# Optimization experiments

Hardware: AMD Instinct MI355X
Metric: run time of the kernel (lower is better)

Reference implementation:

```python
import jax, jax.numpy as jnp
import numpy as np

B, OBS, ACT = 16384, 39, 4
D = 400            # backbone_hidden[-1] == expert_hidden[-1] == task_queries_dim
NE, NT = 8, 10     # num_experts, num_tasks


def setup_inputs() -> dict:
    key = jax.random.key(0)
    ks = jax.random.split(key, 20)
    g = lambda k, shp, fan: jax.random.normal(k, shp, dtype=jnp.float32) / np.sqrt(fan)
    return {
        "obs": jax.random.normal(ks[0], (B, OBS), dtype=jnp.float32),
        "act": jax.random.normal(ks[1], (B, ACT), dtype=jnp.float32),
        "task": jax.random.randint(ks[2], (B,), 0, NT),
        # backbone mlp: [obs+act, 400, 400], relu after each layer
        "bb_w1": g(ks[3], (OBS + ACT, D), OBS + ACT), "bb_b1": jnp.zeros((D,), jnp.float32),
        "bb_w2": g(ks[4], (D, D), D), "bb_b2": jnp.zeros((D,), jnp.float32),
        # 8 expert mlps, stacked: [400 -> 400 -> 400], relu after each layer
        "ex_w1": g(ks[5], (NE, D, D), D), "ex_b1": jnp.zeros((NE, D), jnp.float32),
        "ex_w2": g(ks[6], (NE, D, D), D), "ex_b2": jnp.zeros((NE, D), jnp.float32),
        # attention params
        "key_mat": g(ks[7], (NE, D, D), D),
        "value_mat": g(ks[8], (NE, D, D), D),
        "task_queries": jax.random.normal(ks[9], (NT, D), dtype=jnp.float32),
        # tower mlp: [400, 400, 400, 1], relu on hidden layers, identity output
        "tw_w1": g(ks[10], (D, D), D), "tw_b1": jnp.zeros((D,), jnp.float32),
        "tw_w2": g(ks[11], (D, D), D), "tw_b2": jnp.zeros((D,), jnp.float32),
        "tw_w3": g(ks[12], (D, 1), D), "tw_b3": jnp.zeros((1,), jnp.float32),
    }


def reference(obs, act, task, bb_w1, bb_b1, bb_w2, bb_b2,
              ex_w1, ex_b1, ex_w2, ex_b2,
              key_mat, value_mat, task_queries,
              tw_w1, tw_b1, tw_w2, tw_b2, tw_w3, tw_b3):
    x = jnp.concatenate([obs, act], axis=-1)                       # [B, obs+act]
    h = jax.nn.relu(x @ bb_w1 + bb_b1)
    h = jax.nn.relu(h @ bb_w2 + bb_b2)                             # [B, D]
    # all experts as one batched GEMM: e[n, b, :] = expert_n(h[b])
    e = jax.nn.relu(jnp.einsum('bi,nij->nbj', h, ex_w1) + ex_b1[:, None, :])
    e = jax.nn.relu(jnp.einsum('nbi,nij->nbj', e, ex_w2) + ex_b2[:, None, :])  # [NE, B, D]
    # per-expert key/value projections (einsum 'nij,nj->ni' batched over b)
    vals = jnp.einsum('nij,nbj->bni', value_mat, e)                # [B, NE, D]
    keys = jnp.einsum('nij,nbj->bni', key_mat, e)                  # [B, NE, D]
    q = task_queries[task]                                         # [B, D]
    scores = jnp.einsum('bni,bi->bn', keys, q)                     # [B, NE]
    w = jax.nn.softmax(scores, axis=-1)                            # softmax over experts
    tower_in = jnp.einsum('bn,bni->bi', w, vals)                   # [B, D]
    t = jax.nn.relu(tower_in @ tw_w1 + tw_b1)
    t = jax.nn.relu(t @ tw_w2 + tw_b2)
    qval = t @ tw_w3 + tw_b3                                       # [B, 1]
    return jnp.squeeze(qval, -1)                                   # [B]
```

## Files before the change

### kernel.cpp

```cpp
#include <hip/hip_runtime.h>

typedef _Float16 f16;
typedef f16 f16x8 __attribute__((ext_vector_type(8)));
typedef float f32x4 __attribute__((ext_vector_type(4)));

#define NB 16384
#define D 400
#define DP 416
#define NEXP 8
#define NTASK 10
#define NKT 13

#define MEMFENCE asm volatile("" ::: "memory")
#define BAR() do{ MEMFENCE; __builtin_amdgcn_s_barrier(); MEMFENCE; }while(0)
#define VM(N) asm volatile("s_waitcnt vmcnt(" #N ")" ::: "memory")
#define LGKM0 asm volatile("s_waitcnt lgkmcnt(0)" ::: "memory")

static __device__ __forceinline__ f32x4 mfma16x32(f16x8 a, f16x8 b, f32x4 c){
  return __builtin_amdgcn_mfma_f32_16x16x32_f16(a, b, c, 0, 0, 0);
}
static __device__ __forceinline__ void g2l(const void* g, void* l){
  __builtin_amdgcn_global_load_lds((const __attribute__((address_space(1))) void*)g,
      (__attribute__((address_space(3))) void*)l, 16, 0, 0);
}
static __device__ __forceinline__ f16x8 scale8(f16x8 a, f16 s){
  f16x8 r;
  #pragma unroll
  for (int e=0;e<8;e++) r[e] = a[e]*s;
  return r;
}

static __device__ __forceinline__ void stage_duo(const char* wbase, char* lds, int kt,
                                                 int t0, int dd, int h, int lane){
  const int r = lane >> 3, c = lane & 7, cg = c ^ r;
  g2l(wbase + (size_t)((t0 + dd*2 + (cg>>2))*16 + h*8 + r)*832 + (size_t)kt*64 + (cg&3)*16,
      lds + dd*2048 + h*1024);
}
static __device__ __forceinline__ f16x8 rdB(const f16* buf, int dloc, int t, int lhi, int l15){
  return *(const f16x8*)(buf + dloc*1024 + l15*64 + ((((t*4+lhi) ^ (l15&7)))<<3));
}
static __device__ __forceinline__ f16x8 rdL(const f16* lact, int r, int kt, int lhi){
  int q = kt*4 + lhi;
  int c = (q < 48) ? (q ^ (r&7)) : q;
  return *(const f16x8*)(lact + r*416 + (c<<3));
}
static __device__ __forceinline__ int lact_idx(int r, int col){
  int q = col >> 3;
  int c = (q < 48) ? (q ^ (r&7)) : q;
  return r*416 + (c<<3) + (col&7);
}
static __device__ __forceinline__ void stageB4(const char* wb, char* buf, int kt,
                                               int wv, int lane){
  for (int u = wv; u < 26; u += 4) stage_duo(wb, buf, kt, 0, u>>1, u&1, lane);
}


__global__ void k_build_x(const float* __restrict__ obs, const float* __restrict__ act,
                          f16* __restrict__ x)
{
  int idx = blockIdx.x*256 + threadIdx.x;
  int b = idx >> 6, c = idx & 63;
  float v = 0.f;
  if (c < 39) v = obs[b*39 + c];
  else if (c < 43) v = act[b*4 + (c - 39)];
  x[idx] = (f16)v;
}

__global__ void k_transpose_all(
    const float* __restrict__ bb_w1, const float* __restrict__ bb_w2,
    const float* __restrict__ ex_w1, const float* __restrict__ ex_w2,
    const float* __restrict__ tw_w1, const float* __restrict__ tw_w2,
    f16* __restrict__ bbw1T, f16* __restrict__ bbw2T,
    f16* __restrict__ exw1T, f16* __restrict__ exw2T,
    f16* __restrict__ tw1T,  f16* __restrict__ tw2T)
{
  __shared__ float t[32][33];
  const int z = blockIdx.z;
  const float* in; f16* out; int K = D;
  if (z == 0){ in = bb_w1; out = bbw1T; K = 43; }
  else if (z == 1){ in = bb_w2; out = bbw2T; }
  else if (z < 10){ in = ex_w1 + (size_t)(z-2)*D*D;  out = exw1T + (size_t)(z-2)*DP*DP; }
  else if (z < 18){ in = ex_w2 + (size_t)(z-10)*D*D; out = exw2T + (size_t)(z-10)*DP*DP; }
  else if (z == 18){ in = tw_w1; out = tw1T; }
  else { in = tw_w2; out = tw2T; }
  int tx = threadIdx.x & 31, ty = threadIdx.x >> 5;
  int n0 = blockIdx.x*32, k0 = blockIdx.y*32;
  #pragma unroll
  for (int r=0;r<4;r++){
    int k = k0 + ty + r*8, nn = n0 + tx;
    t[ty + r*8][tx] = (k < K && nn < D) ? in[(size_t)k*D + nn] : 0.f;
  }
  __syncthreads();
  #pragma unroll
  for (int r=0;r<4;r++){
    int nn = n0 + ty + r*8, kp = k0 + tx;
    if (nn < DP && kp < DP) out[(size_t)nn*DP + kp] = (f16)t[tx][ty + r*8];
  }
}

__global__ void k_val_pad(const float* __restrict__ in, f16* __restrict__ out)
{
  int idx = blockIdx.x*256 + threadIdx.x;
  if (idx >= NEXP*DP*DP) return;
  int c = idx % DP, r = (idx / DP) % DP, n = idx / (DP*DP);
  float v = (r < D && c < D) ? in[((size_t)n*D + r)*D + c] : 0.f;
  out[idx] = (f16)v;
}

__global__ void k_kq(const float* __restrict__ key_mat, const float* __restrict__ tq,
                     float* __restrict__ kq)
{
  __shared__ float kcol[D*32];
  __shared__ float tqs[NTASK*D];
  const int n = blockIdx.x, cb = blockIdx.y, tid = threadIdx.x;
  const int c0 = cb*32;
  const float* km = key_mat + (size_t)n*D*D;
  for (int idx=tid; idx<NTASK*D; idx+=256) tqs[idx] = tq[idx];
  for (int idx=tid; idx<D*32; idx+=256){
    int i = idx>>5, c = idx&31;
    int col = c0 + c;
    kcol[idx] = (col < D) ? km[(size_t)i*D + col] : 0.f;
  }
  __syncthreads();
  const int c = tid & 31, tg = tid >> 5;
  #pragma unroll
  for (int rep=0; rep<2; rep++){
    int t = tg + rep*8;
    if (t < NTASK){
      float acc = 0.f;
      for (int i=0;i<D;i++) acc += kcol[i*32+c] * tqs[t*D+i];
      int col = c0 + c;
      if (col < DP) kq[((size_t)n*NTASK + t)*DP + col] = acc;
    }
  }
}


#define MFMA26(a0_, a1_, BUF) do {                                              \
    __builtin_amdgcn_s_setprio(1);                                              \
    _Pragma("unroll")                                                           \
    for (int j=0;j<13;j++){                                                     \
      int tj = ch*13 + j;                                                       \
      f16x8 b = rdB((BUF), tj>>1, tj&1, lhi, l15);                              \
      acc[0][j] = mfma16x32((a0_), b, acc[0][j]);                               \
      acc[1][j] = mfma16x32((a1_), b, acc[1][j]);                               \
    }                                                                           \
    __builtin_amdgcn_s_setprio(0);                                              \
  } while(0)

#define MFMA13(a0_, BUF) do {                                                   \
    __builtin_amdgcn_s_setprio(1);                                              \
    _Pragma("unroll")                                                           \
    for (int j=0;j<13;j++){                                                     \
      int tj = ch*13 + j;                                                       \
      f16x8 b = rdB((BUF), tj>>1, tj&1, lhi, l15);                              \
      acc[j] = mfma16x32((a0_), b, acc[j]);                                     \
    }                                                                           \
    __builtin_amdgcn_s_setprio(0);                                              \
  } while(0)

#define STAGE_W(wb_, buf_, p_, full_) do{                                       \
    int tot_ = (full_) ? 52 : 26;                                               \
    for (int u = wv; u < tot_; u += 4){                                         \
      int kh_ = (u >= 26) ? 1 : 0, uu_ = u - (kh_ ? 26 : 0);                    \
      stage_duo((wb_), (char*)(buf_)[kh_], 2*(p_)+kh_, 0, uu_>>1, uu_&1, lane); \
    }                                                                           \
  } while(0)

__global__ __launch_bounds__(256,2) void k_experts(
    const f16* __restrict__ h16, const f16* __restrict__ w1T, const float* __restrict__ b1s,
    const f16* __restrict__ w2T, const float* __restrict__ b2s,
    f16* __restrict__ e16, const float* __restrict__ kqg, const int* __restrict__ task,
    float* __restrict__ scores)
{
  __shared__ f16 bufB[13*1024];
  __shared__ f16 lact[64*416];
  float (*psum)[2] = (float(*)[2])lact;
  const int tid = threadIdx.x, lane = tid & 63, wv = tid >> 6;
  const int l15 = lane & 15, lhi = lane >> 4;
  const int rh = wv >> 1, ch = wv & 1;
  const int n = blockIdx.x;
  const int rowbase = blockIdx.y * 64;
  const int K0 = ((blockIdx.x + blockIdx.y) & 1) * 7;
  const f32x4 Z4 = {0,0,0,0};
  f32x4 acc[2][13];

  const char* wb1 = (const char*)(w1T + (size_t)n*DP*DP);
  const char* wb2 = (const char*)(w2T + (size_t)n*DP*DP);
  const f16* Ab = h16 + (size_t)(rowbase + rh*32 + l15)*DP;

  #pragma unroll
  for (int j=0;j<13;j++){ acc[0][j]=Z4; acc[1][j]=Z4; }
  f16x8 a0 = *(const f16x8*)(Ab + K0*32 + lhi*8);
  f16x8 a1 = *(const f16x8*)(Ab + 16*DP + K0*32 + lhi*8);
  stageB4(wb1, (char*)bufB, K0, wv, lane);
  for (int kt=0; kt<NKT; kt++){
    VM(0); BAR();
    MFMA26(a0, a1, bufB);
    BAR();
    if (kt < NKT-1){
      int kn = kt + 1 + K0; if (kn >= NKT) kn -= NKT;
      a0 = *(const f16x8*)(Ab + kn*32 + lhi*8);
      a1 = *(const f16x8*)(Ab + 16*DP + kn*32 + lhi*8);
      stageB4(wb1, (char*)bufB, kn, wv, lane);
    }
  }
  stageB4(wb2, (char*)bufB, K0, wv, lane);
  #pragma unroll
  for (int j=0;j<13;j++){
    int col = (ch*13+j)*16 + l15;
    float bv = (col<D)? b1s[n*D+col] : 0.f;
    #pragma unroll
    for (int ar=0;ar<2;ar++)
      #pragma unroll
      for (int rr=0;rr<4;rr++){
        float v = acc[ar][j][rr] + bv; v = v>0.f?v:0.f;
        lact[lact_idx(rh*32+ar*16+lhi*4+rr, col)] = (f16)v;
      }
  }
  LGKM0;

  #pragma unroll
  for (int j=0;j<13;j++){ acc[0][j]=Z4; acc[1][j]=Z4; }
  for (int kt=0; kt<NKT; kt++){
    int ka = kt + K0; if (ka >= NKT) ka -= NKT;
    VM(0); BAR();
    f16x8 x0 = rdL(lact, rh*32 + l15, ka, lhi);
    f16x8 x1 = rdL(lact, rh*32 + 16 + l15, ka, lhi);
    MFMA26(x0, x1, bufB);
    BAR();
    if (kt < NKT-1){
      int kn = kt + 1 + K0; if (kn >= NKT) kn -= NKT;
      stageB4(wb2, (char*)bufB, kn, wv, lane);
    }
  }
  const float* kqp[2][4];
  const float* kqb = kqg + (size_t)n*NTASK*DP;
  #pragma unroll
  for (int ar=0;ar<2;ar++)
    #pragma unroll
    for (int rr=0;rr<4;rr++){
      int grow = rowbase + rh*32 + ar*16 + lhi*4 + rr;
      kqp[ar][rr] = kqb + (size_t)task[grow]*DP;
    }
  float p_[2][4] = {{0,0,0,0},{0,0,0,0}};
  #pragma unroll
  for (int j=0;j<13;j++){
    int col = (ch*13+j)*16 + l15;
    float bv = (col<D)? b2s[n*D+col] : 0.f;
    #pragma unroll
    for (int ar=0;ar<2;ar++)
      #pragma unroll
      for (int rr=0;rr<4;rr++){
        float v = acc[ar][j][rr] + bv; v = v>0.f?v:0.f;
        e16[((size_t)n*NB + rowbase + rh*32+ar*16+lhi*4+rr)*DP + col] = (f16)v;
        p_[ar][rr] += v * kqp[ar][rr][col];
      }
  }
  #pragma unroll
  for (int ar=0;ar<2;ar++)
    #pragma unroll
    for (int rr=0;rr<4;rr++){
      float p = p_[ar][rr];
      p += __shfl_xor(p, 1, 64);
      p += __shfl_xor(p, 2, 64);
      p += __shfl_xor(p, 4, 64);
      p += __shfl_xor(p, 8, 64);
      if (l15 == 0) psum[rh*32+ar*16+lhi*4+rr][ch] = p;
    }
  LGKM0; BAR();
  if (tid < 64) scores[(size_t)(rowbase + tid)*NEXP + n] = psum[tid][0] + psum[tid][1];
}

__global__ __launch_bounds__(256,2) void k_backbone(
    const f16* __restrict__ x, const f16* __restrict__ w1T, const float* __restrict__ b1,
    const f16* __restrict__ w2T, const float* __restrict__ b2, f16* __restrict__ h16)
{
  __shared__ f16 bufB[2][13*1024];
  __shared__ f16 lact[32*416];
  const int tid = threadIdx.x, lane = tid & 63, wv = tid >> 6;
  const int l15 = lane & 15, lhi = lane >> 4;
  const int rh = wv >> 1, ch = wv & 1;
  const int rowbase = blockIdx.x * 32;
  const int P0 = (blockIdx.x & 1) * 3;
  const f32x4 Z4 = {0,0,0,0};
  f32x4 acc[13];

  const f16* Ab = x + (size_t)(rowbase + rh*16 + l15)*64;

  #pragma unroll
  for (int j=0;j<13;j++) acc[j]=Z4;
  STAGE_W((const char*)w1T, bufB, 0, 1);
  f16x8 a0 = *(const f16x8*)(Ab + lhi*8);
  f16x8 a1 = *(const f16x8*)(Ab + 32 + lhi*8);
  VM(0); BAR();
  MFMA13(a0, bufB[0]);
  MFMA13(a1, bufB[1]);
  BAR();
  { int pa0 = P0; STAGE_W((const char*)w2T, bufB, pa0, pa0 != 6); }
  #pragma unroll
  for (int j=0;j<13;j++){
    int col = (ch*13+j)*16 + l15;
    float bv = (col<D)? b1[col] : 0.f;
    #pragma unroll
    for (int rr=0;rr<4;rr++){
      float v = acc[j][rr] + bv; v = v>0.f?v:0.f;
      lact[lact_idx(rh*16+lhi*4+rr, col)] = (f16)v;
    }
  }
  LGKM0;

  #pragma unroll
  for (int j=0;j<13;j++) acc[j]=Z4;
  for (int p=0; p<7; p++){
    int pa = p + P0; if (pa >= 7) pa -= 7;
    VM(0); BAR();
    f16x8 x0 = rdL(lact, rh*16 + l15, 2*pa, lhi);
    MFMA13(x0, bufB[0]);
    if (pa != 6){
      f16x8 x1 = rdL(lact, rh*16 + l15, 2*pa+1, lhi);
      MFMA13(x1, bufB[1]);
    }
    BAR();
    if (p < 6){
      int pn = p + 1 + P0; if (pn >= 7) pn -= 7;
      STAGE_W((const char*)w2T, bufB, pn, pn != 6);
    }
  }
  #pragma unroll
  for (int j=0;j<13;j++){
    int col = (ch*13+j)*16 + l15;
    float bv = (col<D)? b2[col] : 0.f;
    #pragma unroll
    for (int rr=0;rr<4;rr++){
      float v = acc[j][rr] + bv; v = v>0.f?v:0.f;
      h16[(size_t)(rowbase + rh*16+lhi*4+rr)*DP + col] = (f16)v;
    }
  }
}

__global__ __launch_bounds__(256,2) void k_attn(
    const f16* __restrict__ e16, const f16* __restrict__ valT,
    const float* __restrict__ scores, f16* __restrict__ ti16)
{
  __shared__ f16 buf[2][7*1024];
  __shared__ float wsm[64*NEXP];
  const int tid = threadIdx.x, lane = tid & 63, wv = tid >> 6;
  const int l15 = lane & 15, lhi = lane >> 4;
  const int rg = wv >> 1, cg = wv & 1;
  const int cb = blockIdx.x;
  const int rowbase = blockIdx.y * 64;
  const int nd = cb ? 6 : 7;
  const int ntw = cb ? 6 : 7;
  const int t0 = cb * 14;
  const int S0 = ((blockIdx.x + blockIdx.y) & 1) * 28;
  const f32x4 Z4 = {0,0,0,0};
  f32x4 acc[2][7];
  #pragma unroll
  for (int a=0;a<2;a++)
    #pragma unroll
    for (int j=0;j<7;j++) acc[a][j]=Z4;

  if (tid < 64){
    const float* sr = scores + (size_t)(rowbase + tid)*NEXP;
    float s[8]; float m = -1e30f;
    #pragma unroll
    for (int k=0;k<8;k++){ s[k]=sr[k]; m = fmaxf(m, s[k]); }
    float sum = 0.f;
    #pragma unroll
    for (int k=0;k<8;k++){ s[k] = expf(s[k]-m); sum += s[k]; }
    float inv = 1.f/sum;
    #pragma unroll
    for (int k=0;k<8;k++) wsm[tid*NEXP + k] = s[k]*inv;
  }

  #define STAGE_A(n_, p_) do {                                                  \
    const char* vb_ = (const char*)(valT + (size_t)(n_)*DP*DP);                 \
    int nu_ = nd*2, tot_ = ((p_)<6) ? nd*4 : nd*2;                              \
    for (int u = wv; u < tot_; u += 4){                                         \
      int kh_ = (u >= nu_) ? 1 : 0, uu_ = u - (kh_ ? nu_ : 0);                  \
      stage_duo(vb_, (char*)buf[kh_], 2*(p_)+kh_, t0, uu_>>1, uu_&1, lane);     \
    }                                                                           \
  } while(0)

  #define LDA_A(n_, kt_, ar_) \
    (*(const f16x8*)(e16 + ((size_t)(n_)*NB + rowbase + rg*32 + (ar_)*16 + l15)*DP + (kt_)*32 + lhi*8))

  const int nS = S0 / 7;
  STAGE_A(nS, 0);
  f16x8 aC00 = LDA_A(nS,0,0), aC01 = LDA_A(nS,0,1);
  f16x8 aC10 = LDA_A(nS,1,0), aC11 = LDA_A(nS,1,1);
  LGKM0;

  for (int s=0;s<NEXP*7;s++){
    int sa = s + S0; if (sa >= NEXP*7) sa -= NEXP*7;
    int n = sa / 7, p = sa % 7;
    VM(0); BAR();
    f16 w0 = (f16)wsm[(rg*32      + l15)*NEXP + n];
    f16 w1 = (f16)wsm[(rg*32 + 16 + l15)*NEXP + n];
    {
      f16x8 as0 = scale8(aC00, w0), as1 = scale8(aC01, w1);
      __builtin_amdgcn_s_setprio(1);
      #pragma unroll
      for (int j=0;j<7;j++) if (j<ntw){
        int tl = cg*ntw + j;
        f16x8 b = rdB(buf[0], tl>>1, tl&1, lhi, l15);
        acc[0][j] = mfma16x32(as0, b, acc[0][j]);
        acc[1][j] = mfma16x32(as1, b, acc[1][j]);
      }
      __builtin_amdgcn_s_setprio(0);
    }
    if (p < 6){
      f16x8 as0 = scale8(aC10, w0), as1 = scale8(aC11, w1);
      __builtin_amdgcn_s_setprio(1);
      #pragma unroll
      for (int j=0;j<7;j++) if (j<ntw){
        int tl = cg*ntw + j;
        f16x8 b = rdB(buf[1], tl>>1, tl&1, lhi, l15);
        acc[0][j] = mfma16x32(as0, b, acc[0][j]);
        acc[1][j] = mfma16x32(as1, b, acc[1][j]);
      }
      __builtin_amdgcn_s_setprio(0);
    }
    BAR();
    if (s < NEXP*7 - 1){
      int sa2 = sa + 1; if (sa2 >= NEXP*7) sa2 -= NEXP*7;
      int n2 = sa2 / 7, p2 = sa2 % 7;
      STAGE_A(n2, p2);
      aC00 = LDA_A(n2, 2*p2,   0); aC01 = LDA_A(n2, 2*p2,   1);
      if (p2 < 6){ aC10 = LDA_A(n2, 2*p2+1, 0); aC11 = LDA_A(n2, 2*p2+1, 1); }
    }
  }
  #pragma unroll
  for (int ar=0;ar<2;ar++)
    #pragma unroll
    for (int j=0;j<7;j++) if (j<ntw){
      int col = (t0 + cg*ntw + j)*16 + l15;
      #pragma unroll
      for (int rr=0;rr<4;rr++)
        ti16[(size_t)(rowbase + rg*32 + ar*16 + lhi*4 + rr)*DP + col] = (f16)acc[ar][j][rr];
    }
}

__global__ __launch_bounds__(256,2) void k_mlp3(
    const f16* __restrict__ ti16,
    const f16* __restrict__ tw1T, const float* __restrict__ tb1,
    const f16* __restrict__ tw2T, const float* __restrict__ tb2,
    const float* __restrict__ tw3, const float* __restrict__ tb3,
    float* __restrict__ out)
{
  __shared__ f16 bufB[2][13*1024];
  __shared__ f16 lact[32*416];
  float (*psum)[2] = (float(*)[2])lact;
  const int tid = threadIdx.x, lane = tid & 63, wv = tid >> 6;
  const int l15 = lane & 15, lhi = lane >> 4;
  const int rh = wv >> 1, ch = wv & 1;
  const int rowbase = blockIdx.x * 32;
  const int P0 = (blockIdx.x & 1) * 3;
  const f32x4 Z4 = {0,0,0,0};
  f32x4 acc[13];

  const f16* Ab = ti16 + (size_t)(rowbase + rh*16 + l15)*DP;

  #pragma unroll
  for (int j=0;j<13;j++) acc[j]=Z4;
  STAGE_W((const char*)tw1T, bufB, P0, P0 != 6);
  f16x8 a0 = *(const f16x8*)(Ab + (2*P0)*32 + lhi*8);
  f16x8 a1 = (P0 != 6) ? *(const f16x8*)(Ab + (2*P0+1)*32 + lhi*8) : a0;
  for (int p=0; p<7; p++){
    int pa = p + P0; if (pa >= 7) pa -= 7;
    VM(0); BAR();
    MFMA13(a0, bufB[0]);
    if (pa != 6) MFMA13(a1, bufB[1]);
    BAR();
    if (p < 6){
      int pn = p + 1 + P0; if (pn >= 7) pn -= 7;
      STAGE_W((const char*)tw1T, bufB, pn, pn != 6);
      a0 = *(const f16x8*)(Ab + (2*pn)*32 + lhi*8);
      if (pn != 6) a1 = *(const f16x8*)(Ab + (2*pn+1)*32 + lhi*8);
    }
  }
  { int pa0 = P0; STAGE_W((const char*)tw2T, bufB, pa0, pa0 != 6); }
  #pragma unroll
  for (int j=0;j<13;j++){
    int col = (ch*13+j)*16 + l15;
    float bv = (col<D)? tb1[col] : 0.f;
    #pragma unroll
    for (int rr=0;rr<4;rr++){
      float v = acc[j][rr] + bv; v = v>0.f?v:0.f;
      lact[lact_idx(rh*16+lhi*4+rr, col)] = (f16)v;
    }
  }
  LGKM0;

  #pragma unroll
  for (int j=0;j<13;j++) acc[j]=Z4;
  for (int p=0; p<7; p++){
    int pa = p + P0; if (pa >= 7) pa -= 7;
    VM(0); BAR();
    f16x8 x0 = rdL(lact, rh*16 + l15, 2*pa, lhi);
    MFMA13(x0, bufB[0]);
    if (pa != 6){
      f16x8 x1 = rdL(lact, rh*16 + l15, 2*pa+1, lhi);
      MFMA13(x1, bufB[1]);
    }
    BAR();
    if (p < 6){
      int pn = p + 1 + P0; if (pn >= 7) pn -= 7;
      STAGE_W((const char*)tw2T, bufB, pn, pn != 6);
    }
  }
  float p_[4] = {0,0,0,0};
  #pragma unroll
  for (int j=0;j<13;j++){
    int col = (ch*13+j)*16 + l15;
    float bv = (col<D)? tb2[col] : 0.f;
    float w3 = (col<D)? tw3[col] : 0.f;
    #pragma unroll
    for (int rr=0;rr<4;rr++){
      float v = acc[j][rr] + bv; v = v>0.f?v:0.f;
      p_[rr] += v * w3;
    }
  }
  #pragma unroll
  for (int rr=0;rr<4;rr++){
    float p = p_[rr];
    p += __shfl_xor(p, 1, 64);
    p += __shfl_xor(p, 2, 64);
    p += __shfl_xor(p, 4, 64);
    p += __shfl_xor(p, 8, 64);
    if (l15 == 0) psum[rh*16+lhi*4+rr][ch] = p;
  }
  LGKM0; BAR();
  if (tid < 32) out[rowbase + tid] = psum[tid][0] + psum[tid][1] + tb3[0];
}


extern "C" void kernel_launch(void* const* d_in, const int* in_sizes, int n_in,
                              void* d_out, int out_size, void* d_ws, size_t ws_size,
                              hipStream_t stream)
{
  const float* obs     = (const float*)d_in[0];
  const float* act     = (const float*)d_in[1];
  const int*   task    = (const int*)  d_in[2];
  const float* bb_w1   = (const float*)d_in[3];
  const float* bb_b1   = (const float*)d_in[4];
  const float* bb_w2   = (const float*)d_in[5];
  const float* bb_b2   = (const float*)d_in[6];
  const float* ex_w1   = (const float*)d_in[7];
  const float* ex_b1   = (const float*)d_in[8];
  const float* ex_w2   = (const float*)d_in[9];
  const float* ex_b2   = (const float*)d_in[10];
  const float* key_mat = (const float*)d_in[11];
  const float* val_mat = (const float*)d_in[12];
  const float* tq      = (const float*)d_in[13];
  const float* tw_w1   = (const float*)d_in[14];
  const float* tw_b1   = (const float*)d_in[15];
  const float* tw_w2   = (const float*)d_in[16];
  const float* tw_b2   = (const float*)d_in[17];
  const float* tw_w3   = (const float*)d_in[18];
  const float* tw_b3   = (const float*)d_in[19];

  char* ws = (char*)d_ws;
  size_t off = 0;
  auto alloc = [&](size_t bytes){ void* p = ws + off; off += (bytes + 255) & ~(size_t)255; return p; };
  f16*   x16   = (f16*)  alloc((size_t)NB*64*2);
  f16*   h16   = (f16*)  alloc((size_t)NB*DP*2);
  f16*   e16   = (f16*)  alloc((size_t)NEXP*NB*DP*2);
  f16*   ti16  = (f16*)  alloc((size_t)NB*DP*2);
  float* scors = (float*)alloc((size_t)NB*NEXP*4);
  float* kq    = (float*)alloc((size_t)NEXP*NTASK*DP*4);
  f16*   bbw1T = (f16*)  alloc((size_t)DP*DP*2);
  f16*   bbw2T = (f16*)  alloc((size_t)DP*DP*2);
  f16*   exw1T = (f16*)  alloc((size_t)NEXP*DP*DP*2);
  f16*   exw2T = (f16*)  alloc((size_t)NEXP*DP*DP*2);
  f16*   valT  = (f16*)  alloc((size_t)NEXP*DP*DP*2);
  f16*   tw1T  = (f16*)  alloc((size_t)DP*DP*2);
  f16*   tw2T  = (f16*)  alloc((size_t)DP*DP*2);
  (void)ws_size; (void)in_sizes; (void)n_in; (void)out_size;

  k_build_x<<<NB*64/256, 256, 0, stream>>>(obs, act, x16);
  k_transpose_all<<<dim3(13,13,20), 256, 0, stream>>>(
      bb_w1, bb_w2, ex_w1, ex_w2, tw_w1, tw_w2,
      bbw1T, bbw2T, exw1T, exw2T, tw1T, tw2T);
  k_val_pad<<<(NEXP*DP*DP + 255)/256, 256, 0, stream>>>(val_mat, valT);
  k_kq<<<dim3(NEXP, 13), 256, 0, stream>>>(key_mat, tq, kq);

  k_backbone<<<NB/32, 256, 0, stream>>>(x16, bbw1T, bb_b1, bbw2T, bb_b2, h16);
  k_experts<<<dim3(NEXP, NB/64), 256, 0, stream>>>(h16, exw1T, ex_b1, exw2T, ex_b2,
                                                   e16, kq, task, scors);
  k_attn<<<dim3(2, NB/64), 256, 0, stream>>>(e16, valT, scors, ti16);
  k_mlp3<<<NB/32, 256, 0, stream>>>(ti16, tw1T, tw_b1, tw2T, tw_b2, tw_w3, tw_b3,
                                    (float*)d_out);
}
```

Before: 364.1 us.

## Use 512-thread blocks in experts and attention kernels with 16 rows per wave

Doubles the block size of k_experts and k_attn from 256 to 512 threads. Each wave now computes one 16-row MFMA tile instead of two, which halves its accumulator registers. Weight staging is spread over 8 waves. The aim is more waves in flight to hide latency and less register pressure per wave. The cost is that each B fragment read from LDS now feeds half as many MFMAs, and more waves take part in every barrier.

```diff
diff --git a/kernel.cpp b/kernel.cpp
--- a/kernel.cpp
+++ b/kernel.cpp
@@ -52,6 +52,10 @@
 static __device__ __forceinline__ void stageB4(const char* wb, char* buf, int kt,
                                                int wv, int lane){
   for (int u = wv; u < 26; u += 4) stage_duo(wb, buf, kt, 0, u>>1, u&1, lane);
+}
+static __device__ __forceinline__ void stageB8(const char* wb, char* buf, int kt,
+                                               int wv, int lane){
+  for (int u = wv; u < 26; u += 8) stage_duo(wb, buf, kt, 0, u>>1, u&1, lane);
 }
 
 
@@ -136,18 +140,6 @@
 }
 
 
-#define MFMA26(a0_, a1_, BUF) do {                                              \
-    __builtin_amdgcn_s_setprio(1);                                              \
-    _Pragma("unroll")                                                           \
-    for (int j=0;j<13;j++){                                                     \
-      int tj = ch*13 + j;                                                       \
-      f16x8 b = rdB((BUF), tj>>1, tj&1, lhi, l15);                              \
-      acc[0][j] = mfma16x32((a0_), b, acc[0][j]);                               \
-      acc[1][j] = mfma16x32((a1_), b, acc[1][j]);                               \
-    }                                                                           \
-    __builtin_amdgcn_s_setprio(0);                                              \
-  } while(0)
-
 #define MFMA13(a0_, BUF) do {                                                   \
     __builtin_amdgcn_s_setprio(1);                                              \
     _Pragma("unroll")                                                           \
@@ -167,7 +159,7 @@
     }                                                                           \
   } while(0)
 
-__global__ __launch_bounds__(256,2) void k_experts(
+__global__ __launch_bounds__(512,2) void k_experts(
     const f16* __restrict__ h16, const f16* __restrict__ w1T, const float* __restrict__ b1s,
     const f16* __restrict__ w2T, const float* __restrict__ b2s,
     f16* __restrict__ e16, const float* __restrict__ kqg, const int* __restrict__ task,
@@ -183,91 +175,80 @@
   const int rowbase = blockIdx.y * 64;
   const int K0 = ((blockIdx.x + blockIdx.y) & 1) * 7;
   const f32x4 Z4 = {0,0,0,0};
-  f32x4 acc[2][13];
+  f32x4 acc[13];
 
   const char* wb1 = (const char*)(w1T + (size_t)n*DP*DP);
   const char* wb2 = (const char*)(w2T + (size_t)n*DP*DP);
-  const f16* Ab = h16 + (size_t)(rowbase + rh*32 + l15)*DP;
-
-  #pragma unroll
-  for (int j=0;j<13;j++){ acc[0][j]=Z4; acc[1][j]=Z4; }
+  const f16* Ab = h16 + (size_t)(rowbase + rh*16 + l15)*DP;
+
+  #pragma unroll
+  for (int j=0;j<13;j++) acc[j]=Z4;
   f16x8 a0 = *(const f16x8*)(Ab + K0*32 + lhi*8);
-  f16x8 a1 = *(const f16x8*)(Ab + 16*DP + K0*32 + lhi*8);
-  stageB4(wb1, (char*)bufB, K0, wv, lane);
+  stageB8(wb1, (char*)bufB, K0, wv, lane);
   for (int kt=0; kt<NKT; kt++){
     VM(0); BAR();
-    MFMA26(a0, a1, bufB);
+    MFMA13(a0, bufB);
     BAR();
     if (kt < NKT-1){
       int kn = kt + 1 + K0; if (kn >= NKT) kn -= NKT;
       a0 = *(const f16x8*)(Ab + kn*32 + lhi*8);
-      a1 = *(const f16x8*)(Ab + 16*DP + kn*32 + lhi*8);
-      stageB4(wb1, (char*)bufB, kn, wv, lane);
-    }
-  }
-  stageB4(wb2, (char*)bufB, K0, wv, lane);
+      stageB8(wb1, (char*)bufB, kn, wv, lane);
+    }
+  }
+  stageB8(wb2, (char*)bufB, K0, wv, lane);
   #pragma unroll
   for (int j=0;j<13;j++){
     int col = (ch*13+j)*16 + l15;
     float bv = (col<D)? b1s[n*D+col] : 0.f;
     #pragma unroll
-    for (int ar=0;ar<2;ar++)
-      #pragma unroll
-      for (int rr=0;rr<4;rr++){
-        float v = acc[ar][j][rr] + bv; v = v>0.f?v:0.f;
-        lact[lact_idx(rh*32+ar*16+lhi*4+rr, col)] = (f16)v;
-      }
+    for (int rr=0;rr<4;rr++){
+      float v = acc[j][rr] + bv; v = v>0.f?v:0.f;
+      lact[lact_idx(rh*16+lhi*4+rr, col)] = (f16)v;
+    }
   }
   LGKM0;
 
   #pragma unroll
-  for (int j=0;j<13;j++){ acc[0][j]=Z4; acc[1][j]=Z4; }
+  for (int j=0;j<13;j++) acc[j]=Z4;
   for (int kt=0; kt<NKT; kt++){
     int ka = kt + K0; if (ka >= NKT) ka -= NKT;
     VM(0); BAR();
-    f16x8 x0 = rdL(lact, rh*32 + l15, ka, lhi);
-    f16x8 x1 = rdL(lact, rh*32 + 16 + l15, ka, lhi);
-    MFMA26(x0, x1, bufB);
+    f16x8 x0 = rdL(lact, rh*16 + l15, ka, lhi);
+    MFMA13(x0, bufB);
     BAR();
     if (kt < NKT-1){
       int kn = kt + 1 + K0; if (kn >= NKT) kn -= NKT;
-      stageB4(wb2, (char*)bufB, kn, wv, lane);
-    }
-  }
-  const float* kqp[2][4];
+      stageB8(wb2, (char*)bufB, kn, wv, lane);
+    }
+  }
+  const float* kqp[4];
   const float* kqb = kqg + (size_t)n*NTASK*DP;
   #pragma unroll
-  for (int ar=0;ar<2;ar++)
-    #pragma unroll
-    for (int rr=0;rr<4;rr++){
-      int grow = rowbase + rh*32 + ar*16 + lhi*4 + rr;
-      kqp[ar][rr] = kqb + (size_t)task[grow]*DP;
-    }
-  float p_[2][4] = {{0,0,0,0},{0,0,0,0}};
+  for (int rr=0;rr<4;rr++){
+    int grow = rowbase + rh*16 + lhi*4 + rr;
+    kqp[rr] = kqb + (size_t)task[grow]*DP;
+  }
+  float p_[4] = {0,0,0,0};
   #pragma unroll
   for (int j=0;j<13;j++){
     int col = (ch*13+j)*16 + l15;
     float bv = (col<D)? b2s[n*D+col] : 0.f;
     #pragma unroll
-    for (int ar=0;ar<2;ar++)
-      #pragma unroll
-      for (int rr=0;rr<4;rr++){
-        float v = acc[ar][j][rr] + bv; v = v>0.f?v:0.f;
-        e16[((size_t)n*NB + rowbase + rh*32+ar*16+lhi*4+rr)*DP + col] = (f16)v;
-        p_[ar][rr] += v * kqp[ar][rr][col];
-      }
-  }
-  #pragma unroll
-  for (int ar=0;ar<2;ar++)
-    #pragma unroll
     for (int rr=0;rr<4;rr++){
-      float p = p_[ar][rr];
-      p += __shfl_xor(p, 1, 64);
-      p += __shfl_xor(p, 2, 64);
-      p += __shfl_xor(p, 4, 64);
-      p += __shfl_xor(p, 8, 64);
-      if (l15 == 0) psum[rh*32+ar*16+lhi*4+rr][ch] = p;
-    }
+      float v = acc[j][rr] + bv; v = v>0.f?v:0.f;
+      e16[((size_t)n*NB + rowbase + rh*16+lhi*4+rr)*DP + col] = (f16)v;
+      p_[rr] += v * kqp[rr][col];
+    }
+  }
+  #pragma unroll
+  for (int rr=0;rr<4;rr++){
+    float p = p_[rr];
+    p += __shfl_xor(p, 1, 64);
+    p += __shfl_xor(p, 2, 64);
+    p += __shfl_xor(p, 4, 64);
+    p += __shfl_xor(p, 8, 64);
+    if (l15 == 0) psum[rh*16+lhi*4+rr][ch] = p;
+  }
   LGKM0; BAR();
   if (tid < 64) scores[(size_t)(rowbase + tid)*NEXP + n] = psum[tid][0] + psum[tid][1];
 }
@@ -339,7 +320,7 @@
   }
 }
 
-__global__ __launch_bounds__(256,2) void k_attn(
+__global__ __launch_bounds__(512,2) void k_attn(
     const f16* __restrict__ e16, const f16* __restrict__ valT,
     const float* __restrict__ scores, f16* __restrict__ ti16)
 {
@@ -355,11 +336,9 @@
   const int t0 = cb * 14;
   const int S0 = ((blockIdx.x + blockIdx.y) & 1) * 28;
   const f32x4 Z4 = {0,0,0,0};
-  f32x4 acc[2][7];
-  #pragma unroll
-  for (int a=0;a<2;a++)
-    #pragma unroll
-    for (int j=0;j<7;j++) acc[a][j]=Z4;
+  f32x4 acc[7];
+  #pragma unroll
+  for (int j=0;j<7;j++) acc[j]=Z4;
 
   if (tid < 64){
     const float* sr = scores + (size_t)(rowbase + tid)*NEXP;
@@ -377,48 +356,45 @@
   #define STAGE_A(n_, p_) do {                                                  \
     const char* vb_ = (const char*)(valT + (size_t)(n_)*DP*DP);                 \
     int nu_ = nd*2, tot_ = ((p_)<6) ? nd*4 : nd*2;                              \
-    for (int u = wv; u < tot_; u += 4){                                         \
+    for (int u = wv; u < tot_; u += 8){                                         \
       int kh_ = (u >= nu_) ? 1 : 0, uu_ = u - (kh_ ? nu_ : 0);                  \
       stage_duo(vb_, (char*)buf[kh_], 2*(p_)+kh_, t0, uu_>>1, uu_&1, lane);     \
     }                                                                           \
   } while(0)
 
-  #define LDA_A(n_, kt_, ar_) \
-    (*(const f16x8*)(e16 + ((size_t)(n_)*NB + rowbase + rg*32 + (ar_)*16 + l15)*DP + (kt_)*32 + lhi*8))
+  #define LDA_A(n_, kt_) \
+    (*(const f16x8*)(e16 + ((size_t)(n_)*NB + rowbase + rg*16 + l15)*DP + (kt_)*32 + lhi*8))
 
   const int nS = S0 / 7;
   STAGE_A(nS, 0);
-  f16x8 aC00 = LDA_A(nS,0,0), aC01 = LDA_A(nS,0,1);
-  f16x8 aC10 = LDA_A(nS,1,0), aC11 = LDA_A(nS,1,1);
+  f16x8 aC0 = LDA_A(nS,0);
+  f16x8 aC1 = LDA_A(nS,1);
   LGKM0;
 
   for (int s=0;s<NEXP*7;s++){
     int sa = s + S0; if (sa >= NEXP*7) sa -= NEXP*7;
     int n = sa / 7, p = sa % 7;
     VM(0); BAR();
-    f16 w0 = (f16)wsm[(rg*32      + l15)*NEXP + n];
-    f16 w1 = (f16)wsm[(rg*32 + 16 + l15)*NEXP + n];
+    f16 w0 = (f16)wsm[(rg*16 + l15)*NEXP + n];
     {
-      f16x8 as0 = scale8(aC00, w0), as1 = scale8(aC01, w1);
+      f16x8 as0 = scale8(aC0, w0);
       __builtin_amdgcn_s_setprio(1);
       #pragma unroll
       for (int j=0;j<7;j++) if (j<ntw){
         int tl = cg*ntw + j;
         f16x8 b = rdB(buf[0], tl>>1, tl&1, lhi, l15);
-        acc[0][j] = mfma16x32(as0, b, acc[0][j]);
-        acc[1][j] = mfma16x32(as1, b, acc[1][j]);
+        acc[j] = mfma16x32(as0, b, acc[j]);
       }
       __builtin_amdgcn_s_setprio(0);
     }
     if (p < 6){
-      f16x8 as0 = scale8(aC10, w0), as1 = scale8(aC11, w1);
+      f16x8 as1 = scale8(aC1, w0);
       __builtin_amdgcn_s_setprio(1);
       #pragma unroll
       for (int j=0;j<7;j++) if (j<ntw){
         int tl = cg*ntw + j;
         f16x8 b = rdB(buf[1], tl>>1, tl&1, lhi, l15);
-        acc[0][j] = mfma16x32(as0, b, acc[0][j]);
-        acc[1][j] = mfma16x32(as1, b, acc[1][j]);
+        acc[j] = mfma16x32(as1, b, acc[j]);
       }
       __builtin_amdgcn_s_setprio(0);
     }
@@ -427,19 +403,17 @@
       int sa2 = sa + 1; if (sa2 >= NEXP*7) sa2 -= NEXP*7;
       int n2 = sa2 / 7, p2 = sa2 % 7;
       STAGE_A(n2, p2);
-      aC00 = LDA_A(n2, 2*p2,   0); aC01 = LDA_A(n2, 2*p2,   1);
-      if (p2 < 6){ aC10 = LDA_A(n2, 2*p2+1, 0); aC11 = LDA_A(n2, 2*p2+1, 1); }
-    }
-  }
-  #pragma unroll
-  for (int ar=0;ar<2;ar++)
-    #pragma unroll
-    for (int j=0;j<7;j++) if (j<ntw){
-      int col = (t0 + cg*ntw + j)*16 + l15;
-      #pragma unroll
-      for (int rr=0;rr<4;rr++)
-        ti16[(size_t)(rowbase + rg*32 + ar*16 + lhi*4 + rr)*DP + col] = (f16)acc[ar][j][rr];
-    }
+      aC0 = LDA_A(n2, 2*p2);
+      if (p2 < 6) aC1 = LDA_A(n2, 2*p2+1);
+    }
+  }
+  #pragma unroll
+  for (int j=0;j<7;j++) if (j<ntw){
+    int col = (t0 + cg*ntw + j)*16 + l15;
+    #pragma unroll
+    for (int rr=0;rr<4;rr++)
+      ti16[(size_t)(rowbase + rg*16 + lhi*4 + rr)*DP + col] = (f16)acc[j][rr];
+  }
 }
 
 __global__ __launch_bounds__(256,2) void k_mlp3(
@@ -587,9 +561,9 @@
   k_kq<<<dim3(NEXP, 13), 256, 0, stream>>>(key_mat, tq, kq);
 
   k_backbone<<<NB/32, 256, 0, stream>>>(x16, bbw1T, bb_b1, bbw2T, bb_b2, h16);
-  k_experts<<<dim3(NEXP, NB/64), 256, 0, stream>>>(h16, exw1T, ex_b1, exw2T, ex_b2,
+  k_experts<<<dim3(NEXP, NB/64), 512, 0, stream>>>(h16, exw1T, ex_b1, exw2T, ex_b2,
                                                    e16, kq, task, scors);
-  k_attn<<<dim3(2, NB/64), 256, 0, stream>>>(e16, valT, scors, ti16);
+  k_attn<<<dim3(2, NB/64), 512, 0, stream>>>(e16, valT, scors, ti16);
   k_mlp3<<<NB/32, 256, 0, stream>>>(ti16, tw1T, tw_b1, tw2T, tw_b2, tw_w3, tw_b3,
                                     (float*)d_out);
 }
```

After: 431.9 us. +18.6%, slower.
